# Kernel tuning notes

Hardware: AMD Instinct MI355X
Metric: run time of the kernel (lower is better)

The kernel has to match this reference:

```python
import jax, jax.numpy as jnp
import numpy as np

DIM = 2048
NH = 16
HD = DIM // NH          # 128
ROPE = 64               # qk_rope_head_dim
B = 2
S = 2048
LAYER_ID = 12
LAMBDA_INIT = float(0.8 - 0.6 * np.exp(-0.3 * LAYER_ID))
EPS = 1e-5


def _rope(x, cos, sin):
    # interleaved RoPE: pairs (x[2i], x[2i+1]) rotated by angle; x: [b,s,h,ROPE]
    xr = x[..., 0::2]
    xi = x[..., 1::2]
    c = cos[None, :, None, :]  # [1,s,1,ROPE/2]
    s_ = sin[None, :, None, :]
    yr = xr * c - xi * s_
    yi = xr * s_ + xi * c
    return jnp.stack([yr, yi], axis=-1).reshape(x.shape)


def _rope_head(t, cos, sin):
    # apply RoPE to first ROPE dims of head_dim, pass-through the rest
    return jnp.concatenate([_rope(t[..., :ROPE], cos, sin), t[..., ROPE:]], axis=-1)


def setup_inputs() -> dict:
    key = jax.random.key(0)
    ks = jax.random.split(key, 10)
    inner = 2 * NH * HD
    x = jax.random.normal(ks[0], (B, S, DIM), jnp.float32)
    w_q = jax.random.normal(ks[1], (inner, DIM), jnp.float32) * (DIM ** -0.5)
    w_k = jax.random.normal(ks[2], (inner, DIM), jnp.float32) * (DIM ** -0.5)
    w_v = jax.random.normal(ks[3], (inner, DIM), jnp.float32) * (DIM ** -0.5)
    w_o = jax.random.normal(ks[4], (DIM, inner), jnp.float32) * (inner ** -0.5)
    # lambda reparameterization params (paper uses small-std init for stability)
    lambda_q1 = jax.random.normal(ks[5], (NH, HD), jnp.float32) * 0.1
    lambda_k1 = jax.random.normal(ks[6], (NH, HD), jnp.float32) * 0.1
    lambda_q2 = jax.random.normal(ks[7], (NH, HD), jnp.float32) * 0.1
    lambda_k2 = jax.random.normal(ks[8], (NH, HD), jnp.float32) * 0.1
    rms_scale = jnp.ones((NH, 2 * HD), jnp.float32)
    # rotary frequencies
    pos = jnp.arange(S, dtype=jnp.float32)
    inv_freq = 1.0 / (10000.0 ** (jnp.arange(0, ROPE, 2, dtype=jnp.float32) / ROPE))
    ang = pos[:, None] * inv_freq[None, :]  # [S, ROPE/2]
    freqs_cos = jnp.cos(ang)
    freqs_sin = jnp.sin(ang)
    # additive causal mask
    mask = jnp.triu(jnp.full((S, S), -1e9, jnp.float32), k=1)
    return dict(x=x, w_q=w_q, w_k=w_k, w_v=w_v, w_o=w_o,
                lambda_q1=lambda_q1, lambda_k1=lambda_k1,
                lambda_q2=lambda_q2, lambda_k2=lambda_k2,
                rms_scale=rms_scale, freqs_cos=freqs_cos, freqs_sin=freqs_sin,
                mask=mask)


def reference(x, w_q, w_k, w_v, w_o, lambda_q1, lambda_k1, lambda_q2, lambda_k2,
              rms_scale, freqs_cos, freqs_sin, mask):
    b, s, _ = x.shape
    q = (x @ w_q.T).reshape(b, s, NH, 2 * HD)
    k = (x @ w_k.T).reshape(b, s, NH, 2 * HD)
    v = (x @ w_v.T).reshape(b, s, NH, 2 * HD)
    q1, q2 = jnp.split(q, 2, axis=-1)
    k1, k2 = jnp.split(k, 2, axis=-1)
    q1 = _rope_head(q1, freqs_cos, freqs_sin)
    q2 = _rope_head(q2, freqs_cos, freqs_sin)
    k1 = _rope_head(k1, freqs_cos, freqs_sin)
    k2 = _rope_head(k2, freqs_cos, freqs_sin)
    # start_pos = 0 prefill -> cache slice equals current k/v
    scale = HD ** -0.5
    s1 = jnp.einsum('bqhd,bkhd->bhqk', q1, k1) * scale + mask[None, None]
    s2 = jnp.einsum('bqhd,bkhd->bhqk', q2, k2) * scale + mask[None, None]
    a1 = jax.nn.softmax(s1, axis=-1)
    a2 = jax.nn.softmax(s2, axis=-1)
    lam1 = jnp.exp(jnp.sum(lambda_q1 * lambda_k1, axis=-1))  # [NH]
    lam2 = jnp.exp(jnp.sum(lambda_q2 * lambda_k2, axis=-1))
    lam = lam1 - lam2 + LAMBDA_INIT
    attn = a1 - lam[None, :, None, None] * a2
    o = jnp.einsum('bhqk,bkhd->bqhd', attn, v)  # [b,s,NH,2*HD]
    # headwise RMSNorm over 2*head_dim, then (1 - lambda_init) scaling
    o = o * jax.lax.rsqrt(jnp.mean(o * o, axis=-1, keepdims=True) + EPS)
    o = o * rms_scale[None, None] * (1.0 - LAMBDA_INIT)
    return o.reshape(b, s, 2 * NH * HD) @ w_o.T
```

## Files before the change

### kernel.cpp

```cpp
#include <hip/hip_runtime.h>

typedef __attribute__((ext_vector_type(8))) short s16x8;
typedef __attribute__((ext_vector_type(4))) short s16x4;
typedef __attribute__((ext_vector_type(4))) float f32x4;

#define NHh   16
#define Sd    2048
#define Bb    2
#define MSd   4096
#define DIMd  2048
#define INNERd 4096

constexpr float LAMBDA_INIT = 0.7836057665f;
constexpr float POST_SCALE  = 1.0f - LAMBDA_INIT;
constexpr float QK_SCALE    = 0.08838834764831845f;
constexpr float EPSf        = 1e-5f;

__device__ __forceinline__ short f2bf(float x) {
  unsigned u = __builtin_bit_cast(unsigned, x);
  u = (u + 0x7fffu + ((u >> 16) & 1u)) >> 16;
  return (short)u;
}
__device__ __forceinline__ float bf2f(short x) {
  unsigned u = ((unsigned)(unsigned short)x) << 16;
  return __builtin_bit_cast(float, u);
}
__device__ __forceinline__ f32x4 mfma16(s16x8 a, s16x8 b, f32x4 c) {
  return __builtin_amdgcn_mfma_f32_16x16x32_bf16(a, b, c, 0, 0, 0);
}
__device__ __forceinline__ void async16(void* lds, const void* g) {
  __builtin_amdgcn_global_load_lds(
      (const __attribute__((address_space(1))) void*)g,
      (__attribute__((address_space(3))) void*)lds, 16, 0, 0);
}

__global__ __launch_bounds__(256)
void convert5(const float* __restrict__ a0, const float* __restrict__ a1,
              const float* __restrict__ a2, const float* __restrict__ a3,
              const float* __restrict__ a4,
              short* __restrict__ o0, short* __restrict__ o1,
              short* __restrict__ o2, short* __restrict__ o3,
              short* __restrict__ o4) {
  const float* src; short* dst;
  switch (blockIdx.y) {
    case 0: src = a0; dst = o0; break;
    case 1: src = a1; dst = o1; break;
    case 2: src = a2; dst = o2; break;
    case 3: src = a3; dst = o3; break;
    default: src = a4; dst = o4; break;
  }
  size_t i = ((size_t)blockIdx.x * 256 + threadIdx.x) * 4;
  f32x4 x = *(const f32x4*)(src + i);
  s16x4 o;
#pragma unroll
  for (int j = 0; j < 4; ++j) o[j] = f2bf(x[j]);
  *(s16x4*)(dst + i) = o;
}

__global__ void lambda_kernel(const float* __restrict__ lq1, const float* __restrict__ lk1,
                              const float* __restrict__ lq2, const float* __restrict__ lk2,
                              float* __restrict__ lam) {
  int h = threadIdx.x;
  if (h < NHh) {
    float s1 = 0.f, s2 = 0.f;
    for (int d = 0; d < 128; ++d) {
      s1 += lq1[h * 128 + d] * lk1[h * 128 + d];
      s2 += lq2[h * 128 + d] * lk2[h * 128 + d];
    }
    lam[h] = expf(s1) - expf(s2) + LAMBDA_INIT;
  }
}

template <typename OutT>
__global__ __launch_bounds__(256)
void gemm_bt(const short* __restrict__ A, const short* __restrict__ Bm,
             OutT* __restrict__ C, int M, int N, int K) {
  __shared__ __align__(16) short As[128 * 32];
  __shared__ __align__(16) short Bs[128 * 32];
  const int tid  = threadIdx.x;
  const int lane = tid & 63;
  const int w    = tid >> 6;
  const int wr   = (w >> 1) * 64;
  const int wc   = (w & 1) * 64;
  const int m0   = blockIdx.x * 128;
  const int n0   = blockIdx.y * 128;
  const int l15  = lane & 15, l4 = lane >> 4;

  f32x4 acc[4][4] = {};

  for (int kt = 0; kt < K; kt += 32) {
#pragma unroll
    for (int j = 0; j < 2; ++j) {
      int L  = j * 4096 + tid * 16;
      int r  = L >> 6;
      int s  = (L >> 4) & 3;
      int sp = s ^ ((r >> 1) & 3);
      async16((char*)As + L, A  + (size_t)(m0 + r) * K + kt + sp * 8);
      async16((char*)Bs + L, Bm + (size_t)(n0 + r) * K + kt + sp * 8);
    }
    __syncthreads();

    s16x8 af[4], bf[4];
#pragma unroll
    for (int mi = 0; mi < 4; ++mi) {
      int r  = wr + mi * 16 + l15;
      int sl = l4 ^ ((r >> 1) & 3);
      af[mi] = *(const s16x8*)(As + r * 32 + sl * 8);
    }
#pragma unroll
    for (int ni = 0; ni < 4; ++ni) {
      int r  = wc + ni * 16 + l15;
      int sl = l4 ^ ((r >> 1) & 3);
      bf[ni] = *(const s16x8*)(Bs + r * 32 + sl * 8);
    }
#pragma unroll
    for (int mi = 0; mi < 4; ++mi)
#pragma unroll
      for (int ni = 0; ni < 4; ++ni)
        acc[mi][ni] = mfma16(af[mi], bf[ni], acc[mi][ni]);
    __syncthreads();
  }

#pragma unroll
  for (int mi = 0; mi < 4; ++mi)
#pragma unroll
    for (int ni = 0; ni < 4; ++ni)
#pragma unroll
      for (int j = 0; j < 4; ++j) {
        int row = m0 + wr + mi * 16 + l4 * 4 + j;
        int col = n0 + wc + ni * 16 + l15;
        float v = acc[mi][ni][j];
        if constexpr (sizeof(OutT) == 2) C[(size_t)row * N + col] = f2bf(v);
        else                             C[(size_t)row * N + col] = v;
      }
}

__global__ __launch_bounds__(256)
void rope_qk(short* __restrict__ qp, short* __restrict__ kp,
             const float* __restrict__ fc, const float* __restrict__ fs) {
  int idx  = blockIdx.x * 256 + threadIdx.x;
  int ib   = idx & 7;
  int half = (idx >> 3) & 1;
  int h    = (idx >> 4) & 15;
  int s    = (idx >> 8) & 2047;
  int b    = (idx >> 19) & 1;
  short* base = (idx >> 20) ? kp : qp;
  size_t off  = ((size_t)(b * Sd + s) * NHh + h) * 256 + half * 128 + ib * 8;
  s16x8 v = *(s16x8*)(base + off);
  f32x4 c  = *(const f32x4*)(fc + s * 32 + ib * 4);
  f32x4 sn = *(const f32x4*)(fs + s * 32 + ib * 4);
#pragma unroll
  for (int p = 0; p < 4; ++p) {
    float xr = bf2f(v[2 * p]), xi = bf2f(v[2 * p + 1]);
    float yr = xr * c[p] - xi * sn[p];
    float yi = xr * sn[p] + xi * c[p];
    v[2 * p]     = f2bf(yr);
    v[2 * p + 1] = f2bf(yi);
  }
  *(s16x8*)(base + off) = v;
}

__global__ __launch_bounds__(256)
void transpose_v(const short* __restrict__ v, short* __restrict__ vt) {
  __shared__ __align__(16) short t[64][80];
  const int s0 = blockIdx.x * 64;
  const int d0 = blockIdx.y * 64;
  const int bh = blockIdx.z;
  const int b  = bh >> 4, h = bh & 15;
  const int tid = threadIdx.x;
#pragma unroll
  for (int rp = 0; rp < 2; ++rp) {
    int i  = rp * 256 + tid;
    int sl = i >> 3;
    int dl = (i & 7) * 8;
    s16x8 x = *(const s16x8*)(v + ((size_t)(b * Sd + s0 + sl) * NHh + h) * 256 + d0 + dl);
    *(s16x8*)(&t[sl][dl]) = x;
  }
  __syncthreads();
#pragma unroll
  for (int rp = 0; rp < 2; ++rp) {
    int i   = rp * 256 + tid;
    int dl  = i >> 3;
    int sp8 = (i & 7) * 8;
    s16x8 x;
#pragma unroll
    for (int j = 0; j < 8; ++j) x[j] = t[sp8 + j][dl];
    *(s16x8*)(vt + ((size_t)bh * 256 + d0 + dl) * Sd + s0 + sp8) = x;
  }
}

__global__ __launch_bounds__(256)
void flash_diff(const short* __restrict__ q, const short* __restrict__ k,
                const short* __restrict__ vt, const float* __restrict__ lam,
                const float* __restrict__ rms_scale, short* __restrict__ obuf) {
  const int qt = blockIdx.x, h = blockIdx.y, b = blockIdx.z;
  const int tid = threadIdx.x;
  const int lane = tid & 63, w = tid >> 6;
  const int q0 = qt * 64;
  const int wrow0 = q0 + w * 16;
  const int l15 = lane & 15, l4 = lane >> 4;

  __shared__ __align__(16) short K1s[32 * 128];
  __shared__ __align__(16) short K2s[32 * 128];
  __shared__ __align__(16) short Vs[256 * 32];
  __shared__ __align__(16) short Ps[4][2][512];

  s16x8 q1f[4], q2f[4];
  {
    const size_t qrow = ((size_t)(b * Sd + wrow0 + l15) * NHh + h) * 256;
#pragma unroll
    for (int kb = 0; kb < 4; ++kb) {
      q1f[kb] = *(const s16x8*)(q + qrow + kb * 32 + l4 * 8);
      q2f[kb] = *(const s16x8*)(q + qrow + 128 + kb * 32 + l4 * 8);
    }
  }

  float m1[4], l1[4], m2[4], l2[4];
#pragma unroll
  for (int j = 0; j < 4; ++j) { m1[j] = m2[j] = -1e30f; l1[j] = l2[j] = 0.f; }
  f32x4 O1[16] = {};
  f32x4 O2[16] = {};

  const int kv_end = q0 + 64;
  for (int kv0 = 0; kv0 < kv_end; kv0 += 32) {
#pragma unroll
    for (int j = 0; j < 2; ++j) {
      int L  = j * 4096 + tid * 16;
      int r  = L >> 8;
      int s  = (L >> 4) & 15;
      int sp = s ^ (r & 7);
      const size_t krow = ((size_t)(b * Sd + kv0 + r) * NHh + h) * 256;
      async16((char*)K1s + L, k + krow + sp * 8);
      async16((char*)K2s + L, k + krow + 128 + sp * 8);
    }
#pragma unroll
    for (int j = 0; j < 4; ++j) {
      int L  = j * 4096 + tid * 16;
      int r  = L >> 6;
      int s  = (L >> 4) & 3;
      int sp = s ^ ((r >> 1) & 3);
      async16((char*)Vs + L, vt + ((size_t)(b * NHh + h) * 256 + r) * Sd + kv0 + sp * 8);
    }
    __syncthreads();

    if (kv0 <= wrow0 + 15) {
      f32x4 s1[2] = {}, s2[2] = {};
#pragma unroll
      for (int kb = 0; kb < 4; ++kb)
#pragma unroll
        for (int cf = 0; cf < 2; ++cf) {
          int r  = cf * 16 + l15;
          int sl = (kb * 4 + l4) ^ (r & 7);
          s16x8 kf1 = *(const s16x8*)(K1s + r * 128 + sl * 8);
          s16x8 kf2 = *(const s16x8*)(K2s + r * 128 + sl * 8);
          s1[cf] = mfma16(q1f[kb], kf1, s1[cf]);
          s2[cf] = mfma16(q2f[kb], kf2, s2[cf]);
        }

      float sv1[2][4], sv2[2][4];
#pragma unroll
      for (int cf = 0; cf < 2; ++cf)
#pragma unroll
        for (int j = 0; j < 4; ++j) {
          int kvc = kv0 + cf * 16 + l15;
          int row = wrow0 + l4 * 4 + j;
          bool msk = kvc > row;
          sv1[cf][j] = msk ? -1e9f : s1[cf][j] * QK_SCALE;
          sv2[cf][j] = msk ? -1e9f : s2[cf][j] * QK_SCALE;
        }

      auto online = [&](float (&sv)[2][4], float (&m)[4], float (&l)[4],
                        f32x4 (&O)[16], short* pbuf) {
        float tmax[4], rs[4], ps[4];
#pragma unroll
        for (int j = 0; j < 4; ++j) tmax[j] = fmaxf(sv[0][j], sv[1][j]);
#pragma unroll
        for (int j = 0; j < 4; ++j) {
          tmax[j] = fmaxf(tmax[j], __shfl_xor(tmax[j], 1));
          tmax[j] = fmaxf(tmax[j], __shfl_xor(tmax[j], 2));
          tmax[j] = fmaxf(tmax[j], __shfl_xor(tmax[j], 4));
          tmax[j] = fmaxf(tmax[j], __shfl_xor(tmax[j], 8));
        }
#pragma unroll
        for (int j = 0; j < 4; ++j) {
          float mn = fmaxf(m[j], tmax[j]);
          rs[j] = __expf(m[j] - mn);
          m[j] = mn;
          ps[j] = 0.f;
        }
#pragma unroll
        for (int cf = 0; cf < 2; ++cf)
#pragma unroll
          for (int j = 0; j < 4; ++j) {
            float p = __expf(sv[cf][j] - m[j]);
            ps[j] += p;
            pbuf[(l4 * 4 + j) * 32 + cf * 16 + l15] = f2bf(p);
          }
#pragma unroll
        for (int j = 0; j < 4; ++j) {
          ps[j] += __shfl_xor(ps[j], 1);
          ps[j] += __shfl_xor(ps[j], 2);
          ps[j] += __shfl_xor(ps[j], 4);
          ps[j] += __shfl_xor(ps[j], 8);
          l[j] = l[j] * rs[j] + ps[j];
        }
#pragma unroll
        for (int nf = 0; nf < 16; ++nf) {
          O[nf][0] *= rs[0]; O[nf][1] *= rs[1];
          O[nf][2] *= rs[2]; O[nf][3] *= rs[3];
        }
      };
      online(sv1, m1, l1, O1, &Ps[w][0][0]);
      online(sv2, m2, l2, O2, &Ps[w][1][0]);

      s16x8 pa1 = *(const s16x8*)(&Ps[w][0][0] + l15 * 32 + l4 * 8);
      s16x8 pa2 = *(const s16x8*)(&Ps[w][1][0] + l15 * 32 + l4 * 8);
#pragma unroll
      for (int nf = 0; nf < 16; ++nf) {
        int d  = nf * 16 + l15;
        int sl = l4 ^ ((d >> 1) & 3);
        s16x8 vf = *(const s16x8*)(Vs + d * 32 + sl * 8);
        O1[nf] = mfma16(pa1, vf, O1[nf]);
        O2[nf] = mfma16(pa2, vf, O2[nf]);
      }
    }
    __syncthreads();
  }

  const float lamh = lam[h];
  float inv1[4], inv2[4], ss[4];
#pragma unroll
  for (int j = 0; j < 4; ++j) {
    inv1[j] = 1.f / l1[j];
    inv2[j] = 1.f / l2[j];
    ss[j] = 0.f;
  }
#pragma unroll
  for (int nf = 0; nf < 16; ++nf)
#pragma unroll
    for (int j = 0; j < 4; ++j) {
      float o = O1[nf][j] * inv1[j] - lamh * O2[nf][j] * inv2[j];
      O1[nf][j] = o;
      ss[j] += o * o;
    }
#pragma unroll
  for (int j = 0; j < 4; ++j) {
    ss[j] += __shfl_xor(ss[j], 1);
    ss[j] += __shfl_xor(ss[j], 2);
    ss[j] += __shfl_xor(ss[j], 4);
    ss[j] += __shfl_xor(ss[j], 8);
    ss[j] = rsqrtf(ss[j] * (1.f / 256.f) + EPSf);
  }
#pragma unroll
  for (int nf = 0; nf < 16; ++nf) {
    float sc = rms_scale[h * 256 + nf * 16 + l15] * POST_SCALE;
#pragma unroll
    for (int j = 0; j < 4; ++j) {
      float v = O1[nf][j] * ss[j] * sc;
      obuf[((size_t)(b * Sd + wrow0 + l4 * 4 + j) * NHh + h) * 256 + nf * 16 + l15] = f2bf(v);
    }
  }
}

extern "C" void kernel_launch(void* const* d_in, const int* in_sizes, int n_in,
                              void* d_out, int out_size, void* d_ws, size_t ws_size,
                              hipStream_t stream) {
  const float* x   = (const float*)d_in[0];
  const float* w_q = (const float*)d_in[1];
  const float* w_k = (const float*)d_in[2];
  const float* w_v = (const float*)d_in[3];
  const float* w_o = (const float*)d_in[4];
  const float* lq1 = (const float*)d_in[5];
  const float* lk1 = (const float*)d_in[6];
  const float* lq2 = (const float*)d_in[7];
  const float* lk2 = (const float*)d_in[8];
  const float* rms = (const float*)d_in[9];
  const float* fc  = (const float*)d_in[10];
  const float* fs  = (const float*)d_in[11];

  char* ws = (char*)d_ws;
  const size_t SMb = 16777216ull;
  const size_t BGb = 33554432ull;
  short* xb  = (short*)(ws);
  short* wqb = (short*)(ws + 1 * SMb);
  short* wkb = (short*)(ws + 2 * SMb);
  short* wvb = (short*)(ws + 3 * SMb);
  short* wob = (short*)(ws + 4 * SMb);
  short* qb  = (short*)(ws + 5 * SMb);
  short* kb  = (short*)(ws + 5 * SMb + 1 * BGb);
  short* vb  = (short*)(ws + 5 * SMb + 2 * BGb);
  short* vtb = (short*)(ws + 5 * SMb + 3 * BGb);
  short* ob  = (short*)(ws + 5 * SMb + 4 * BGb);
  float* lam = (float*)(ws + 5 * SMb + 5 * BGb);

  convert5<<<dim3(8192, 5), 256, 0, stream>>>(x, w_q, w_k, w_v, w_o,
                                              xb, wqb, wkb, wvb, wob);
  lambda_kernel<<<1, 64, 0, stream>>>(lq1, lk1, lq2, lk2, lam);
  gemm_bt<short><<<dim3(32, 32), 256, 0, stream>>>(xb, wqb, qb, 4096, 4096, 2048);
  gemm_bt<short><<<dim3(32, 32), 256, 0, stream>>>(xb, wkb, kb, 4096, 4096, 2048);
  gemm_bt<short><<<dim3(32, 32), 256, 0, stream>>>(xb, wvb, vb, 4096, 4096, 2048);
  rope_qk<<<8192, 256, 0, stream>>>(qb, kb, fc, fs);
  transpose_v<<<dim3(32, 4, 32), 256, 0, stream>>>(vb, vtb);
  flash_diff<<<dim3(32, 16, 2), 256, 0, stream>>>(qb, kb, vtb, lam, rms, ob);
  gemm_bt<float><<<dim3(32, 16), 256, 0, stream>>>(ob, wob, (float*)d_out, 4096, 2048, 4096);
}
```

Baseline: 1.373 ms.

## Split differential attention into per-softmax flash blocks plus combine kernel, swizzle GEMM tiles

The fused two-softmax flash kernel is split so each block handles one of the two attention maps, which doubles the grid and halves register pressure (one O accumulator instead of two). Query tiles are launched in reverse order so the long causal tiles start first, and a padded P buffer stride reduces LDS bank conflicts. A separate combine kernel applies lambda, the headwise RMSNorm and the scaling, at the cost of an extra bf16 round trip of both outputs through global memory. GEMM block indices are remapped with an XCD-style swizzle to improve L2 locality.

```diff
diff --git a/kernel.cpp b/kernel.cpp
--- a/kernel.cpp
+++ b/kernel.cpp
@@ -82,8 +82,14 @@
   const int w    = tid >> 6;
   const int wr   = (w >> 1) * 64;
   const int wc   = (w & 1) * 64;
-  const int m0   = blockIdx.x * 128;
-  const int n0   = blockIdx.y * 128;
+
+  const int nb  = gridDim.x * gridDim.y;
+  const int id  = blockIdx.y * gridDim.x + blockIdx.x;
+  const int cpx = nb >> 3;
+  const int sw  = (id & 7) * cpx + (id >> 3);
+  const int m0  = (sw % gridDim.x) * 128;
+  const int n0  = (sw / gridDim.x) * 128;
+
   const int l15  = lane & 15, l4 = lane >> 4;
 
   f32x4 acc[4][4] = {};
@@ -190,36 +196,35 @@
 }
 
 __global__ __launch_bounds__(256)
-void flash_diff(const short* __restrict__ q, const short* __restrict__ k,
-                const short* __restrict__ vt, const float* __restrict__ lam,
-                const float* __restrict__ rms_scale, short* __restrict__ obuf) {
-  const int qt = blockIdx.x, h = blockIdx.y, b = blockIdx.z;
+void flash_one(const short* __restrict__ q, const short* __restrict__ k,
+               const short* __restrict__ vt,
+               short* __restrict__ o1b, short* __restrict__ o2b) {
+  const int qt  = gridDim.x - 1 - blockIdx.x;
+  const int h   = blockIdx.y >> 1;
+  const int mat = blockIdx.y & 1;
+  const int b   = blockIdx.z;
   const int tid = threadIdx.x;
   const int lane = tid & 63, w = tid >> 6;
   const int q0 = qt * 64;
   const int wrow0 = q0 + w * 16;
   const int l15 = lane & 15, l4 = lane >> 4;
 
-  __shared__ __align__(16) short K1s[32 * 128];
-  __shared__ __align__(16) short K2s[32 * 128];
+  __shared__ __align__(16) short Ks[32 * 128];
   __shared__ __align__(16) short Vs[256 * 32];
-  __shared__ __align__(16) short Ps[4][2][512];
-
-  s16x8 q1f[4], q2f[4];
+  __shared__ __align__(16) short Ps[4][16 * 40];
+
+  s16x8 qf[4];
   {
-    const size_t qrow = ((size_t)(b * Sd + wrow0 + l15) * NHh + h) * 256;
-#pragma unroll
-    for (int kb = 0; kb < 4; ++kb) {
-      q1f[kb] = *(const s16x8*)(q + qrow + kb * 32 + l4 * 8);
-      q2f[kb] = *(const s16x8*)(q + qrow + 128 + kb * 32 + l4 * 8);
-    }
-  }
-
-  float m1[4], l1[4], m2[4], l2[4];
-#pragma unroll
-  for (int j = 0; j < 4; ++j) { m1[j] = m2[j] = -1e30f; l1[j] = l2[j] = 0.f; }
-  f32x4 O1[16] = {};
-  f32x4 O2[16] = {};
+    const size_t qrow = ((size_t)(b * Sd + wrow0 + l15) * NHh + h) * 256 + mat * 128;
+#pragma unroll
+    for (int kb = 0; kb < 4; ++kb)
+      qf[kb] = *(const s16x8*)(q + qrow + kb * 32 + l4 * 8);
+  }
+
+  float m[4], l[4];
+#pragma unroll
+  for (int j = 0; j < 4; ++j) { m[j] = -1e30f; l[j] = 0.f; }
+  f32x4 O[16] = {};
 
   const int kv_end = q0 + 64;
   for (int kv0 = 0; kv0 < kv_end; kv0 += 32) {
@@ -229,9 +234,8 @@
       int r  = L >> 8;
       int s  = (L >> 4) & 15;
       int sp = s ^ (r & 7);
-      const size_t krow = ((size_t)(b * Sd + kv0 + r) * NHh + h) * 256;
-      async16((char*)K1s + L, k + krow + sp * 8);
-      async16((char*)K2s + L, k + krow + 128 + sp * 8);
+      async16((char*)Ks + L,
+              k + ((size_t)(b * Sd + kv0 + r) * NHh + h) * 256 + mat * 128 + sp * 8);
     }
 #pragma unroll
     for (int j = 0; j < 4; ++j) {
@@ -244,122 +248,128 @@
     __syncthreads();
 
     if (kv0 <= wrow0 + 15) {
-      f32x4 s1[2] = {}, s2[2] = {};
+      f32x4 s[2] = {};
 #pragma unroll
       for (int kb = 0; kb < 4; ++kb)
 #pragma unroll
         for (int cf = 0; cf < 2; ++cf) {
           int r  = cf * 16 + l15;
           int sl = (kb * 4 + l4) ^ (r & 7);
-          s16x8 kf1 = *(const s16x8*)(K1s + r * 128 + sl * 8);
-          s16x8 kf2 = *(const s16x8*)(K2s + r * 128 + sl * 8);
-          s1[cf] = mfma16(q1f[kb], kf1, s1[cf]);
-          s2[cf] = mfma16(q2f[kb], kf2, s2[cf]);
+          s16x8 kf = *(const s16x8*)(Ks + r * 128 + sl * 8);
+          s[cf] = mfma16(qf[kb], kf, s[cf]);
         }
 
-      float sv1[2][4], sv2[2][4];
+      float sv[2][4];
 #pragma unroll
       for (int cf = 0; cf < 2; ++cf)
 #pragma unroll
         for (int j = 0; j < 4; ++j) {
           int kvc = kv0 + cf * 16 + l15;
           int row = wrow0 + l4 * 4 + j;
-          bool msk = kvc > row;
-          sv1[cf][j] = msk ? -1e9f : s1[cf][j] * QK_SCALE;
-          sv2[cf][j] = msk ? -1e9f : s2[cf][j] * QK_SCALE;
+          sv[cf][j] = (kvc > row) ? -1e9f : s[cf][j] * QK_SCALE;
         }
 
-      auto online = [&](float (&sv)[2][4], float (&m)[4], float (&l)[4],
-                        f32x4 (&O)[16], short* pbuf) {
-        float tmax[4], rs[4], ps[4];
-#pragma unroll
-        for (int j = 0; j < 4; ++j) tmax[j] = fmaxf(sv[0][j], sv[1][j]);
+      float tmax[4], rs[4], ps[4];
+#pragma unroll
+      for (int j = 0; j < 4; ++j) tmax[j] = fmaxf(sv[0][j], sv[1][j]);
+#pragma unroll
+      for (int j = 0; j < 4; ++j) {
+        tmax[j] = fmaxf(tmax[j], __shfl_xor(tmax[j], 1));
+        tmax[j] = fmaxf(tmax[j], __shfl_xor(tmax[j], 2));
+        tmax[j] = fmaxf(tmax[j], __shfl_xor(tmax[j], 4));
+        tmax[j] = fmaxf(tmax[j], __shfl_xor(tmax[j], 8));
+      }
+#pragma unroll
+      for (int j = 0; j < 4; ++j) {
+        float mn = fmaxf(m[j], tmax[j]);
+        rs[j] = __expf(m[j] - mn);
+        m[j] = mn;
+        ps[j] = 0.f;
+      }
+#pragma unroll
+      for (int cf = 0; cf < 2; ++cf)
 #pragma unroll
         for (int j = 0; j < 4; ++j) {
-          tmax[j] = fmaxf(tmax[j], __shfl_xor(tmax[j], 1));
-          tmax[j] = fmaxf(tmax[j], __shfl_xor(tmax[j], 2));
-          tmax[j] = fmaxf(tmax[j], __shfl_xor(tmax[j], 4));
-          tmax[j] = fmaxf(tmax[j], __shfl_xor(tmax[j], 8));
+          float p = __expf(sv[cf][j] - m[j]);
+          ps[j] += p;
+          Ps[w][(l4 * 4 + j) * 40 + cf * 16 + l15] = f2bf(p);
         }
 #pragma unroll
-        for (int j = 0; j < 4; ++j) {
-          float mn = fmaxf(m[j], tmax[j]);
-          rs[j] = __expf(m[j] - mn);
-          m[j] = mn;
-          ps[j] = 0.f;
-        }
-#pragma unroll
-        for (int cf = 0; cf < 2; ++cf)
-#pragma unroll
-          for (int j = 0; j < 4; ++j) {
-            float p = __expf(sv[cf][j] - m[j]);
-            ps[j] += p;
-            pbuf[(l4 * 4 + j) * 32 + cf * 16 + l15] = f2bf(p);
-          }
-#pragma unroll
-        for (int j = 0; j < 4; ++j) {
-          ps[j] += __shfl_xor(ps[j], 1);
-          ps[j] += __shfl_xor(ps[j], 2);
-          ps[j] += __shfl_xor(ps[j], 4);
-          ps[j] += __shfl_xor(ps[j], 8);
-          l[j] = l[j] * rs[j] + ps[j];
-        }
-#pragma unroll
-        for (int nf = 0; nf < 16; ++nf) {
-          O[nf][0] *= rs[0]; O[nf][1] *= rs[1];
-          O[nf][2] *= rs[2]; O[nf][3] *= rs[3];
-        }
-      };
-      online(sv1, m1, l1, O1, &Ps[w][0][0]);
-      online(sv2, m2, l2, O2, &Ps[w][1][0]);
-
-      s16x8 pa1 = *(const s16x8*)(&Ps[w][0][0] + l15 * 32 + l4 * 8);
-      s16x8 pa2 = *(const s16x8*)(&Ps[w][1][0] + l15 * 32 + l4 * 8);
+      for (int j = 0; j < 4; ++j) {
+        ps[j] += __shfl_xor(ps[j], 1);
+        ps[j] += __shfl_xor(ps[j], 2);
+        ps[j] += __shfl_xor(ps[j], 4);
+        ps[j] += __shfl_xor(ps[j], 8);
+        l[j] = l[j] * rs[j] + ps[j];
+      }
+#pragma unroll
+      for (int nf = 0; nf < 16; ++nf) {
+        O[nf][0] *= rs[0]; O[nf][1] *= rs[1];
+        O[nf][2] *= rs[2]; O[nf][3] *= rs[3];
+      }
+
+      s16x8 pa = *(const s16x8*)(&Ps[w][0] + l15 * 40 + l4 * 8);
 #pragma unroll
       for (int nf = 0; nf < 16; ++nf) {
         int d  = nf * 16 + l15;
         int sl = l4 ^ ((d >> 1) & 3);
         s16x8 vf = *(const s16x8*)(Vs + d * 32 + sl * 8);
-        O1[nf] = mfma16(pa1, vf, O1[nf]);
-        O2[nf] = mfma16(pa2, vf, O2[nf]);
+        O[nf] = mfma16(pa, vf, O[nf]);
       }
     }
     __syncthreads();
   }
 
+  float inv[4];
+#pragma unroll
+  for (int j = 0; j < 4; ++j) inv[j] = 1.f / l[j];
+  short* dst = mat ? o2b : o1b;
+#pragma unroll
+  for (int nf = 0; nf < 16; ++nf)
+#pragma unroll
+    for (int j = 0; j < 4; ++j)
+      dst[((size_t)(b * Sd + wrow0 + l4 * 4 + j) * NHh + h) * 256 + nf * 16 + l15] =
+          f2bf(O[nf][j] * inv[j]);
+}
+
+__global__ __launch_bounds__(256)
+void combine(const short* __restrict__ o1b, const short* __restrict__ o2b,
+             const float* __restrict__ lam, const float* __restrict__ rms,
+             short* __restrict__ ob) {
+  const int t = threadIdx.x;
+  const int row = blockIdx.x * 16 + (t >> 4);
+  const int h = row & 15;
+  const int d0 = (t & 15) * 16;
+  const size_t base = (size_t)row * 256 + d0;
   const float lamh = lam[h];
-  float inv1[4], inv2[4], ss[4];
-#pragma unroll
-  for (int j = 0; j < 4; ++j) {
-    inv1[j] = 1.f / l1[j];
-    inv2[j] = 1.f / l2[j];
-    ss[j] = 0.f;
-  }
-#pragma unroll
-  for (int nf = 0; nf < 16; ++nf)
-#pragma unroll
-    for (int j = 0; j < 4; ++j) {
-      float o = O1[nf][j] * inv1[j] - lamh * O2[nf][j] * inv2[j];
-      O1[nf][j] = o;
-      ss[j] += o * o;
-    }
-#pragma unroll
-  for (int j = 0; j < 4; ++j) {
-    ss[j] += __shfl_xor(ss[j], 1);
-    ss[j] += __shfl_xor(ss[j], 2);
-    ss[j] += __shfl_xor(ss[j], 4);
-    ss[j] += __shfl_xor(ss[j], 8);
-    ss[j] = rsqrtf(ss[j] * (1.f / 256.f) + EPSf);
-  }
-#pragma unroll
-  for (int nf = 0; nf < 16; ++nf) {
-    float sc = rms_scale[h * 256 + nf * 16 + l15] * POST_SCALE;
-#pragma unroll
-    for (int j = 0; j < 4; ++j) {
-      float v = O1[nf][j] * ss[j] * sc;
-      obuf[((size_t)(b * Sd + wrow0 + l4 * 4 + j) * NHh + h) * 256 + nf * 16 + l15] = f2bf(v);
-    }
-  }
+
+  s16x8 a0 = *(const s16x8*)(o1b + base);
+  s16x8 a1 = *(const s16x8*)(o1b + base + 8);
+  s16x8 b0 = *(const s16x8*)(o2b + base);
+  s16x8 b1 = *(const s16x8*)(o2b + base + 8);
+  float o[16];
+  float ss = 0.f;
+#pragma unroll
+  for (int j = 0; j < 8; ++j) {
+    o[j]     = bf2f(a0[j]) - lamh * bf2f(b0[j]);
+    o[8 + j] = bf2f(a1[j]) - lamh * bf2f(b1[j]);
+  }
+#pragma unroll
+  for (int j = 0; j < 16; ++j) ss += o[j] * o[j];
+  ss += __shfl_xor(ss, 1);
+  ss += __shfl_xor(ss, 2);
+  ss += __shfl_xor(ss, 4);
+  ss += __shfl_xor(ss, 8);
+  const float r = rsqrtf(ss * (1.f / 256.f) + EPSf);
+
+  s16x8 w0, w1;
+#pragma unroll
+  for (int j = 0; j < 8; ++j) {
+    w0[j] = f2bf(o[j]     * r * rms[h * 256 + d0 + j]     * POST_SCALE);
+    w1[j] = f2bf(o[8 + j] * r * rms[h * 256 + d0 + 8 + j] * POST_SCALE);
+  }
+  *(s16x8*)(ob + base)     = w0;
+  *(s16x8*)(ob + base + 8) = w1;
 }
 
 extern "C" void kernel_launch(void* const* d_in, const int* in_sizes, int n_in,
@@ -392,6 +402,8 @@
   short* vtb = (short*)(ws + 5 * SMb + 3 * BGb);
   short* ob  = (short*)(ws + 5 * SMb + 4 * BGb);
   float* lam = (float*)(ws + 5 * SMb + 5 * BGb);
+  short* o1b = ob;
+  short* o2b = (short*)(ws);
 
   convert5<<<dim3(8192, 5), 256, 0, stream>>>(x, w_q, w_k, w_v, w_o,
                                               xb, wqb, wkb, wvb, wob);
@@ -401,6 +413,7 @@
   gemm_bt<short><<<dim3(32, 32), 256, 0, stream>>>(xb, wvb, vb, 4096, 4096, 2048);
   rope_qk<<<8192, 256, 0, stream>>>(qb, kb, fc, fs);
   transpose_v<<<dim3(32, 4, 32), 256, 0, stream>>>(vb, vtb);
-  flash_diff<<<dim3(32, 16, 2), 256, 0, stream>>>(qb, kb, vtb, lam, rms, ob);
+  flash_one<<<dim3(32, 32, 2), 256, 0, stream>>>(qb, kb, vtb, o1b, o2b);
+  combine<<<4096, 256, 0, stream>>>(o1b, o2b, lam, rms, ob);
   gemm_bt<float><<<dim3(32, 16), 256, 0, stream>>>(ob, wob, (float*)d_out, 4096, 2048, 4096);
 }
```

New measurement: 1.201 ms. 1.14x faster.
